# Kernel optimization log

Measured on AMD Instinct MI355X. Metric: run time of the kernel, lower is better.

The kernel has to match this reference:

```python
import jax, jax.numpy as jnp
import numpy as np

N = 50000      # nodes
E = 800000     # edges (avg degree 16)
B = 8          # graphs in batch
HID = 64       # hidden channels
NCLS = 40
EPS = 1e-5     # BatchNorm eps


def _init(key, shape, fan_in):
    return jax.random.normal(key, shape, dtype=jnp.float32) / np.sqrt(fan_in)


def setup_inputs() -> dict:
    key = jax.random.key(0)
    ks = jax.random.split(key, 12)
    d = {}
    d["x"] = jax.random.normal(ks[0], (N, 3), jnp.float32)
    d["pos"] = jax.random.normal(ks[1], (N, 3), jnp.float32)
    d["edge_attr"] = jax.random.normal(ks[2], (E,), jnp.float32)
    d["edge_index"] = jax.random.randint(ks[3], (2, E), 0, N, dtype=jnp.int32)
    d["batch"] = jnp.sort(jax.random.randint(ks[4], (N,), 0, B, dtype=jnp.int32))
    # conv1 MLP: input = edge_attr(1) + (x_j - x_i)(6) + x_i(6) = 13, two Lin->ReLU->BN blocks
    d1 = 13
    d["c1_W0"] = _init(ks[5], (d1, HID), d1); d["c1_b0"] = jnp.zeros((HID,), jnp.float32)
    d["c1_g0"] = jnp.ones((HID,), jnp.float32); d["c1_be0"] = jnp.zeros((HID,), jnp.float32)
    d["c1_W1"] = _init(ks[6], (HID, HID), HID); d["c1_b1"] = jnp.zeros((HID,), jnp.float32)
    d["c1_g1"] = jnp.ones((HID,), jnp.float32); d["c1_be1"] = jnp.zeros((HID,), jnp.float32)
    # 3 CustomEdgeConvWeighted layers, MLP input = 2*(3+HID) = 134; stacked over layer dim
    L = 3; dw = 2 * (3 + HID)
    d["cw_W0"] = _init(ks[7], (L, dw, HID), dw); d["cw_b0"] = jnp.zeros((L, HID), jnp.float32)
    d["cw_g0"] = jnp.ones((L, HID), jnp.float32); d["cw_be0"] = jnp.zeros((L, HID), jnp.float32)
    d["cw_W1"] = _init(ks[8], (L, HID, HID), HID); d["cw_b1"] = jnp.zeros((L, HID), jnp.float32)
    d["cw_g1"] = jnp.ones((L, HID), jnp.float32); d["cw_be1"] = jnp.zeros((L, HID), jnp.float32)
    # classifier head: jump-cat of 4 pooled layer outputs -> 4*HID
    d["lin1_W"] = _init(ks[9], (4 * HID, HID), 4 * HID); d["lin1_b"] = jnp.zeros((HID,), jnp.float32)
    d["lin2_W"] = _init(ks[10], (HID, NCLS), HID); d["lin2_b"] = jnp.zeros((NCLS,), jnp.float32)
    return d


def _mlp_layer(h, W, b, g, be):
    # Lin -> ReLU -> BatchNorm1d (training-mode batch stats)
    h = jax.nn.relu(h @ W + b)
    mu = h.mean(axis=0)
    var = h.var(axis=0)
    return (h - mu) * jax.lax.rsqrt(var + EPS) * g + be


def _edge_conv(x, pos, src, dst, extra, p0, p1):
    xc = jnp.concatenate([pos, x], axis=1)        # [N, 3+C]
    xi = xc[dst]                                   # target features  [E, 3+C]
    xj = xc[src]                                   # source features  [E, 3+C]
    parts = [xj - xi, xi]
    if extra is not None:
        parts = [extra] + parts                    # cat([edge_attr, x_j - x_i, x_i])
    m = jnp.concatenate(parts, axis=-1)
    m = _mlp_layer(m, *p0)
    m = _mlp_layer(m, *p1)
    agg = jax.ops.segment_max(m, dst, num_segments=N)  # scatter-max aggregation
    return jnp.where(jnp.isfinite(agg), agg, 0.0)      # isolated nodes -> 0


def _mean_pool(x, batch):
    s = jax.ops.segment_sum(x, batch, num_segments=B)
    cnt = jax.ops.segment_sum(jnp.ones((x.shape[0],), x.dtype), batch, num_segments=B)
    return s / jnp.maximum(cnt, 1.0)[:, None]


def reference(x, pos, edge_attr, edge_index, batch,
              c1_W0, c1_b0, c1_g0, c1_be0, c1_W1, c1_b1, c1_g1, c1_be1,
              cw_W0, cw_b0, cw_g0, cw_be0, cw_W1, cw_b1, cw_g1, cw_be1,
              lin1_W, lin1_b, lin2_W, lin2_b):
    src, dst = edge_index[0], edge_index[1]
    h = jax.nn.relu(_edge_conv(x, pos, src, dst, edge_attr[:, None],
                               (c1_W0, c1_b0, c1_g0, c1_be0),
                               (c1_W1, c1_b1, c1_g1, c1_be1)))
    xs = [_mean_pool(h, batch)]
    for l in range(3):  # fixed small layer count
        h = jax.nn.relu(_edge_conv(h, pos, src, dst, None,
                                   (cw_W0[l], cw_b0[l], cw_g0[l], cw_be0[l]),
                                   (cw_W1[l], cw_b1[l], cw_g1[l], cw_be1[l])))
        xs.append(_mean_pool(h, batch))
    j = jnp.concatenate(xs, axis=-1)               # JumpingKnowledge 'cat' -> [B, 4*HID]
    z = jax.nn.relu(j @ lin1_W + lin1_b) @ lin2_W + lin2_b
    return jax.nn.log_softmax(z, axis=-1)
```

## Files before the change

### kernel.cpp

```cpp
#include <hip/hip_runtime.h>

#define EPSV 1e-5f

typedef __attribute__((ext_vector_type(8))) short bf16x8;
typedef __attribute__((ext_vector_type(4))) float f32x4;

__device__ inline unsigned short f2bf(float f){
    unsigned u = __float_as_uint(f);
    u += 0x7fffu + ((u >> 16) & 1u);
    return (unsigned short)(u >> 16);
}
__device__ inline float bf2f(unsigned short v){
    return __uint_as_float(((unsigned)v) << 16);
}
__device__ inline unsigned cvtpk(float a, float b){
    unsigned r;
    asm("v_cvt_pk_bf16_f32 %0, %1, %2" : "=v"(r) : "v"(a), "v"(b));
    return r;
}


__global__ void k_init(int* deg, int* cursor, int N, int* counters,
                       float* stats, int statsN, float* pool, int poolN,
                       float* nmax, int* src_pad, float* ea_pad, int G16){
    int total = max(N*64, G16);
    for (int i = blockIdx.x*blockDim.x + threadIdx.x; i < total; i += gridDim.x*blockDim.x){
        if (i < N*64) nmax[i] = 0.f;
        if (i < G16){ src_pad[i] = 0; ea_pad[i] = 0.f; }
        if (i < N){ deg[i] = 0; cursor[i] = 0; }
        if (i < 8) counters[i] = 0;
        if (i < statsN) stats[i] = 0.f;
        if (i < poolN)  pool[i]  = 0.f;
    }
}

__global__ void k_hist(const int* dst, int E, int* deg){
    for (int e = blockIdx.x*blockDim.x + threadIdx.x; e < E; e += gridDim.x*blockDim.x)
        atomicAdd(&deg[dst[e]], 1);
}

__global__ __launch_bounds__(256) void k_alloc(const int* __restrict__ deg, int N,
        int* __restrict__ gstart, int* counters){
    int lane = threadIdx.x & 63;
    for (int n = blockIdx.x*blockDim.x + threadIdx.x; n - lane < N; n += gridDim.x*blockDim.x){
        int d = (n < N) ? deg[n] : 0;
        int g = (d + 15) >> 4;
        int sg = g;
        for (int off = 1; off < 64; off <<= 1){
            int tg = __shfl_up(sg, off);
            if (lane >= off) sg += tg;
        }
        int bg = 0;
        if (lane == 63) bg = atomicAdd(&counters[1], sg);
        bg = __shfl(bg, 63);
        if (n < N) gstart[n] = bg + sg - g;
    }
}

__global__ void k_grpfill(const int* deg, const int* gstart, int N,
                          unsigned* grp_nv, const int* counters){
    if (blockIdx.x == 0 && threadIdx.x < 16)
        grp_nv[counters[1] + threadIdx.x] = 0u;
    for (int n = blockIdx.x*blockDim.x + threadIdx.x; n < N; n += gridDim.x*blockDim.x){
        int dg = deg[n];
        int g0 = gstart[n];
        int ng = (dg + 15) >> 4;
        for (int j = 0; j < ng; j++)
            grp_nv[g0 + j] = (unsigned)((n << 5) | min(dg - j*16, 16));
    }
}

__global__ void k_scatter(const int* src, const int* dst, const float* ea, int E,
                          const int* gstart, int* cursor, int* src_c, float* ea_c){
    for (int e = blockIdx.x*blockDim.x + threadIdx.x; e < E; e += gridDim.x*blockDim.x){
        int d = dst[e];
        int p = gstart[d]*16 + atomicAdd(&cursor[d], 1);
        src_c[p] = src[e];
        ea_c[p] = ea[e];
    }
}

__global__ void k_bounds(const int* batch, int N, int B, int* bstart){
    for (int n = blockIdx.x*blockDim.x + threadIdx.x; n < N; n += gridDim.x*blockDim.x){
        if (n == 0){ int b0 = batch[0]; for (int bb = 0; bb <= b0; bb++) bstart[bb] = 0; }
        int b1 = batch[n];
        int b2 = (n + 1 < N) ? batch[n + 1] : B;
        for (int bb = b1 + 1; bb <= b2; bb++) bstart[bb] = n + 1;
    }
}

__global__ __launch_bounds__(256) void k_fold(const float* __restrict__ sum0,
        const float* __restrict__ sq0, float invE,
        const float* __restrict__ g0, const float* __restrict__ be0,
        const float* __restrict__ W1f, const float* __restrict__ b1,
        unsigned short* __restrict__ w1sT, float* __restrict__ badd){
    __shared__ float a0s[64], c0s[64];
    int t = threadIdx.x;
    if (t < 64){
        float m = sum0[t]*invE;
        float v = fmaxf(sq0[t]*invE - m*m, 0.f);
        float r = rsqrtf(v + EPSV);
        float a = g0[t]*r;
        a0s[t] = a; c0s[t] = be0[t] - m*a;
    }
    __syncthreads();
    for (int i = t; i < 4096; i += 256){
        int n = i >> 6, k = i & 63;
        w1sT[i] = f2bf(a0s[k] * W1f[k*64 + n]);
    }
    if (t < 64){
        float acc = b1[t];
        for (int k = 0; k < 64; k++) acc = fmaf(c0s[k], W1f[k*64 + t], acc);
        badd[t] = acc;
    }
}


__global__ __launch_bounds__(256) void k_nodeproj(const float* __restrict__ pos,
        const float* __restrict__ feat, int F, const float* __restrict__ W,
        int ra, int rb, const float* __restrict__ b0,
        unsigned short* __restrict__ P, unsigned short* __restrict__ Q, int N){
    __shared__ float sWa[67*64];
    __shared__ float sWd[67*64];
    int D = 3 + F;
    for (int i = threadIdx.x; i < D*64; i += 256){
        int k = i >> 6, c = i & 63;
        float wa = W[(ra + k)*64 + c];
        sWa[i] = wa;
        sWd[i] = W[(rb + k)*64 + c] - wa;
    }
    __syncthreads();
    int lane = threadIdx.x & 63;
    int wid = (blockIdx.x*256 + threadIdx.x) >> 6;
    int nw  = (gridDim.x*256) >> 6;
    float bb = b0[lane];
    for (int n = wid; n < N; n += nw){
        float p = 0.f, q = 0.f;
        for (int k = 0; k < 3; k++){
            float v = pos[n*3 + k];
            p = fmaf(v, sWa[k*64 + lane], p);
            q = fmaf(v, sWd[k*64 + lane], q);
        }
        for (int k = 0; k < F; k++){
            float v = feat[n*F + k];
            p = fmaf(v, sWa[(3+k)*64 + lane], p);
            q = fmaf(v, sWd[(3+k)*64 + lane], q);
        }
        P[(size_t)n*64 + lane] = f2bf(p);
        Q[(size_t)n*64 + lane] = f2bf(q + bb);
    }
}

#define UNPACK_ADD(up, uq, pre0, pre1) \
    pre0 = __uint_as_float((up) << 16) + __uint_as_float((uq) << 16); \
    pre1 = __uint_as_float((up) & 0xffff0000u) + __uint_as_float((uq) & 0xffff0000u);

template<bool EA>
__global__ __launch_bounds__(256, 3) void k_statsA(const unsigned short* __restrict__ Pb,
        const unsigned short* __restrict__ Qb,
        const int* __restrict__ src_c, const float* __restrict__ ea_c,
        const float* __restrict__ w0e,
        const unsigned* __restrict__ grp_nv, const int* __restrict__ counters,
        float* sum0, float* sq0){
    int lane = threadIdx.x & 63;
    int lo = lane & 15, hi = lane >> 4;
    int wid = (blockIdx.x*256 + threadIdx.x) >> 6;
    int nwv = (gridDim.x*256) >> 6;
    float w0v[16];
    if (EA){
#pragma unroll
        for (int j = 0; j < 8; j++){
            w0v[j]   = w0e[hi*8 + j];
            w0v[8+j] = w0e[32 + hi*8 + j];
        }
    }
    float st1[16], st2[16];
#pragma unroll
    for (int j = 0; j < 16; j++){ st1[j] = 0.f; st2[j] = 0.f; }

    int NG = counters[1];
    int C  = (NG + nwv - 1) / nwv;
    int gw0 = wid * C;
    int cnum = min(C, NG - gw0);
    if (cnum > 0){
        unsigned mr[8]; int sr[8]; float er[8];
        uint4 pa[4], pb[4], qa[4], qb[4];
#pragma unroll
        for (int k = 0; k < 8; k++){
            int G = gw0 + k;
            mr[k] = grp_nv[G];
            sr[k] = src_c[(size_t)G*16 + lo];
            if (EA) er[k] = ea_c[(size_t)G*16 + lo];
        }
#pragma unroll
        for (int d = 0; d < 4; d++){
            const uint4* P4 = (const uint4*)(Pb + (size_t)sr[d]*64);
            const uint4* Q4 = (const uint4*)(Qb + (size_t)(mr[d] >> 5)*64);
            pa[d] = P4[hi]; pb[d] = P4[4+hi]; qa[d] = Q4[hi]; qb[d] = Q4[4+hi];
        }
        int itmax = (cnum + 7) & ~7;
        for (int it = 0; it < itmax; it += 8){
#pragma unroll
            for (int j = 0; j < 8; j++){
                int G = gw0 + it + j;
                unsigned mv = mr[j];
                float eav_all = EA ? er[j] : 0.f;
                int vcv = (it + j < cnum) ? (int)(mv & 31u) : 0;
                mr[j] = grp_nv[G + 8];
                sr[j] = src_c[(size_t)(G + 8)*16 + lo];
                if (EA) er[j] = ea_c[(size_t)(G + 8)*16 + lo];
                int d = j & 3;
                uint4 cpa = pa[d], cpb = pb[d], cqa = qa[d], cqb = qb[d];
                {
                    int s4 = sr[(j+4)&7]; unsigned m4 = mr[(j+4)&7];
                    const uint4* P4 = (const uint4*)(Pb + (size_t)s4*64);
                    const uint4* Q4 = (const uint4*)(Qb + (size_t)(m4 >> 5)*64);
                    pa[d] = P4[hi]; pb[d] = P4[4+hi]; qa[d] = Q4[hi]; qb[d] = Q4[4+hi];
                }
                bool vv = lo < vcv;
                float eav = (EA && vv) ? eav_all : 0.f;
#pragma unroll
                for (int w = 0; w < 4; w++){
                    float pre0, pre1;
                    UNPACK_ADD(((const unsigned*)&cpa)[w], ((const unsigned*)&cqa)[w], pre0, pre1);
                    if (EA){ pre0 = fmaf(eav, w0v[2*w], pre0); pre1 = fmaf(eav, w0v[2*w+1], pre1); }
                    float h0f = vv ? fmaxf(pre0, 0.f) : 0.f;
                    float h1f = vv ? fmaxf(pre1, 0.f) : 0.f;
                    st1[2*w]   += h0f; st2[2*w]   = fmaf(h0f, h0f, st2[2*w]);
                    st1[2*w+1] += h1f; st2[2*w+1] = fmaf(h1f, h1f, st2[2*w+1]);
                    UNPACK_ADD(((const unsigned*)&cpb)[w], ((const unsigned*)&cqb)[w], pre0, pre1);
                    if (EA){ pre0 = fmaf(eav, w0v[8+2*w], pre0); pre1 = fmaf(eav, w0v[8+2*w+1], pre1); }
                    h0f = vv ? fmaxf(pre0, 0.f) : 0.f;
                    h1f = vv ? fmaxf(pre1, 0.f) : 0.f;
                    st1[8+2*w]   += h0f; st2[8+2*w]   = fmaf(h0f, h0f, st2[8+2*w]);
                    st1[8+2*w+1] += h1f; st2[8+2*w+1] = fmaf(h1f, h1f, st2[8+2*w+1]);
                }
            }
        }
    }
#pragma unroll
    for (int m = 1; m < 16; m <<= 1){
#pragma unroll
        for (int j = 0; j < 16; j++){
            st1[j] += __shfl_xor(st1[j], m);
            st2[j] += __shfl_xor(st2[j], m);
        }
    }
    __shared__ float red[4*128];
    int w = threadIdx.x >> 6;
    if (lo == 0){
#pragma unroll
        for (int j = 0; j < 8; j++){
            red[w*128 + hi*8 + j]        = st1[j];
            red[w*128 + 32 + hi*8 + j]   = st1[8+j];
            red[w*128 + 64 + hi*8 + j]   = st2[j];
            red[w*128 + 96 + hi*8 + j]   = st2[8+j];
        }
    }
    __syncthreads();
    int t = threadIdx.x;
    if (t < 128){
        float v = red[t] + red[128 + t] + red[256 + t] + red[384 + t];
        if (t < 64) atomicAdd(&sum0[t], v);
        else        atomicAdd(&sq0[t - 64], v);
    }
}

template<bool EA>
__global__ __launch_bounds__(256, 2) void k_passB2(
        const unsigned short* __restrict__ Pb, const unsigned short* __restrict__ Qb,
        const int* __restrict__ src_c, const float* __restrict__ ea_c,
        const float* __restrict__ w0e,
        const unsigned* __restrict__ grp_nv, const int* __restrict__ counters,
        const unsigned short* __restrict__ w1sT, const float* __restrict__ badd,
        float* nmax, float* sum1, float* sq1){
    int lane = threadIdx.x & 63;
    int lo = lane & 15, hi = lane >> 4;
    int wid = (blockIdx.x*256 + threadIdx.x) >> 6;
    int nwv = (gridDim.x*256) >> 6;

    float w0v[16];
    if (EA){
#pragma unroll
        for (int j = 0; j < 8; j++){
            w0v[j]   = w0e[hi*8 + j];
            w0v[8+j] = w0e[32 + hi*8 + j];
        }
    }
    bf16x8 bfr[2][4];
#pragma unroll
    for (int ks = 0; ks < 2; ks++)
#pragma unroll
        for (int nt = 0; nt < 4; nt++)
            bfr[ks][nt] = *(const bf16x8*)(w1sT + (size_t)(nt*16 + lo)*64 + ks*32 + hi*8);
    float baddv[4];
#pragma unroll
    for (int nt = 0; nt < 4; nt++) baddv[nt] = badd[nt*16 + lo];

    float st1[4] = {0.f,0.f,0.f,0.f}, st2[4] = {0.f,0.f,0.f,0.f};
    int NG = counters[1];
    int C  = (NG + nwv - 1) / nwv;
    int gw0 = wid * C;
    int cnum = min(C, NG - gw0);
    if (cnum > 0){
        unsigned mr[8]; int sr[8]; float er[8];
        uint4 pa[4], pb[4], qa[4], qb[4];
#pragma unroll
        for (int k = 0; k < 8; k++){
            int G = gw0 + k;
            mr[k] = grp_nv[G];
            sr[k] = src_c[(size_t)G*16 + lo];
            if (EA) er[k] = ea_c[(size_t)G*16 + lo];
        }
#pragma unroll
        for (int d = 0; d < 4; d++){
            const uint4* P4 = (const uint4*)(Pb + (size_t)sr[d]*64);
            const uint4* Q4 = (const uint4*)(Qb + (size_t)(mr[d] >> 5)*64);
            pa[d] = P4[hi]; pb[d] = P4[4+hi]; qa[d] = Q4[hi]; qb[d] = Q4[4+hi];
        }
        int itmax = (cnum + 7) & ~7;
        for (int it = 0; it < itmax; it += 8){
#pragma unroll
            for (int j = 0; j < 8; j++){
                int G = gw0 + it + j;
                unsigned mv = mr[j];
                float eav_all = EA ? er[j] : 0.f;
                int vcv = (it + j < cnum) ? (int)(mv & 31u) : 0;
                mr[j] = grp_nv[G + 8];
                sr[j] = src_c[(size_t)(G + 8)*16 + lo];
                if (EA) er[j] = ea_c[(size_t)(G + 8)*16 + lo];
                int d = j & 3;
                uint4 cpa = pa[d], cpb = pb[d], cqa = qa[d], cqb = qb[d];
                {
                    int s4 = sr[(j+4)&7]; unsigned m4 = mr[(j+4)&7];
                    const uint4* P4 = (const uint4*)(Pb + (size_t)s4*64);
                    const uint4* Q4 = (const uint4*)(Qb + (size_t)(m4 >> 5)*64);
                    pa[d] = P4[hi]; pb[d] = P4[4+hi]; qa[d] = Q4[hi]; qb[d] = Q4[4+hi];
                }
                if (vcv > 0){
                    bool vv = lo < vcv;
                    float eav = (EA && vv) ? eav_all : 0.f;
                    bf16x8 af0, af1;
#pragma unroll
                    for (int w = 0; w < 4; w++){
                        float pre0, pre1;
                        UNPACK_ADD(((const unsigned*)&cpa)[w], ((const unsigned*)&cqa)[w], pre0, pre1);
                        if (EA){ pre0 = fmaf(eav, w0v[2*w], pre0); pre1 = fmaf(eav, w0v[2*w+1], pre1); }
                        ((unsigned*)&af0)[w] = cvtpk(fmaxf(pre0, 0.f), fmaxf(pre1, 0.f));
                        UNPACK_ADD(((const unsigned*)&cpb)[w], ((const unsigned*)&cqb)[w], pre0, pre1);
                        if (EA){ pre0 = fmaf(eav, w0v[8+2*w], pre0); pre1 = fmaf(eav, w0v[8+2*w+1], pre1); }
                        ((unsigned*)&af1)[w] = cvtpk(fmaxf(pre0, 0.f), fmaxf(pre1, 0.f));
                    }
                    f32x4 acc[4];
#pragma unroll
                    for (int nt = 0; nt < 4; nt++){
                        acc[nt] = (f32x4){0.f, 0.f, 0.f, 0.f};
                        acc[nt] = __builtin_amdgcn_mfma_f32_16x16x32_bf16(af0, bfr[0][nt], acc[nt], 0, 0, 0);
                        acc[nt] = __builtin_amdgcn_mfma_f32_16x16x32_bf16(af1, bfr[1][nt], acc[nt], 0, 0, 0);
                    }
                    int n = (int)(mv >> 5);
#pragma unroll
                    for (int nt = 0; nt < 4; nt++){
                        float m = 0.f;
#pragma unroll
                        for (int r = 0; r < 4; r++){
                            float h = ((hi*4 + r) < vcv) ? fmaxf(acc[nt][r] + baddv[nt], 0.f) : 0.f;
                            st1[nt] += h;
                            st2[nt] = fmaf(h, h, st2[nt]);
                            m = fmaxf(m, h);
                        }
                        m = fmaxf(m, __shfl_xor(m, 16));
                        m = fmaxf(m, __shfl_xor(m, 32));
                        if (lane < 16)
                            atomicMax((unsigned int*)&nmax[(size_t)n*64 + nt*16 + lane], __float_as_uint(m));
                    }
                }
            }
        }
    }
#pragma unroll
    for (int nt = 0; nt < 4; nt++){
        st1[nt] += __shfl_xor(st1[nt], 16); st1[nt] += __shfl_xor(st1[nt], 32);
        st2[nt] += __shfl_xor(st2[nt], 16); st2[nt] += __shfl_xor(st2[nt], 32);
    }
    __shared__ float red[4*128];
    int w = threadIdx.x >> 6;
    if (lane < 16){
#pragma unroll
        for (int nt = 0; nt < 4; nt++){
            red[w*128 + nt*16 + lane]      = st1[nt];
            red[w*128 + 64 + nt*16 + lane] = st2[nt];
        }
    }
    __syncthreads();
    int t = threadIdx.x;
    if (t < 128){
        float v = red[t] + red[128 + t] + red[256 + t] + red[384 + t];
        if (t < 64) atomicAdd(&sum1[t], v);
        else        atomicAdd(&sq1[t - 64], v);
    }
}

template<bool PROJ>
__global__ __launch_bounds__(256) void k_finproj(float* __restrict__ nmax,
        const int* __restrict__ deg,
        const float* __restrict__ sum1, const float* __restrict__ sq1, float invE,
        const float* __restrict__ g1, const float* __restrict__ be1,
        const int* __restrict__ batch,
        const float* __restrict__ pos, const float* __restrict__ W, const float* __restrict__ b0n,
        unsigned short* __restrict__ P, unsigned short* __restrict__ Q,
        float* pooll, int N, int B){
    __shared__ float sWa[67*64];
    __shared__ float sWd[67*64];
    if (PROJ){
        for (int i = threadIdx.x; i < 67*64; i += 256){
            int k = i >> 6, c = i & 63;
            float wa = W[k*64 + c];
            sWa[i] = wa;
            sWd[i] = W[(67 + k)*64 + c] - wa;
        }
        __syncthreads();
    }
    int lane = threadIdx.x & 63;
    float m1 = sum1[lane]*invE;
    float v1 = fmaxf(sq1[lane]*invE - m1*m1, 0.f);
    float r1 = rsqrtf(v1 + EPSV);
    float av = g1[lane]*r1;
    float cv = be1[lane] - m1*av;
    float bb = PROJ ? b0n[lane] : 0.f;
    int wid = (blockIdx.x*256 + threadIdx.x) >> 6;
    int nw  = (gridDim.x*256) >> 6;
    int chunk = (N + nw - 1) / nw;
    int n0 = wid * chunk, n1 = min(n0 + chunk, N);
    int rep = wid & 7;
    float run = 0.f; int curb = -1;
    for (int n = n0; n < n1; n++){
        size_t idx = (size_t)n*64 + lane;
        float mv = nmax[idx];
        nmax[idx] = 0.f;
        float val = (deg[n] > 0) ? fmaxf(fmaf(av, mv, cv), 0.f) : 0.f;
        int b = batch[n];
        if (b != curb){
            if (curb >= 0) atomicAdd(&pooll[(rep*B + curb)*64 + lane], run);
            run = 0.f; curb = b;
        }
        run += val;
        if (PROJ){
            float p = 0.f, q = 0.f;
            for (int k = 0; k < 3; k++){
                float v = pos[n*3 + k];
                p = fmaf(v, sWa[k*64 + lane], p);
                q = fmaf(v, sWd[k*64 + lane], q);
            }
#pragma unroll
            for (int k = 0; k < 64; k++){
                float v = __shfl(val, k);
                p = fmaf(v, sWa[(3+k)*64 + lane], p);
                q = fmaf(v, sWd[(3+k)*64 + lane], q);
            }
            P[idx] = f2bf(p);
            Q[idx] = f2bf(q + bb);
        }
    }
    if (curb >= 0) atomicAdd(&pooll[(rep*B + curb)*64 + lane], run);
}

__global__ __launch_bounds__(512) void k_head(const float* __restrict__ pool, const int* __restrict__ bstart,
        const float* __restrict__ l1W, const float* __restrict__ l1b,
        const float* __restrict__ l2W, const float* __restrict__ l2b,
        float* __restrict__ out, int B, int NCLS){
    __shared__ float js[8*256];
    __shared__ float z1[8*64];
    __shared__ float zs[8*40];
    int t = threadIdx.x;
    for (int i = t; i < B*256; i += 512){
        int b = i >> 8, k = i & 255;
        int l = k >> 6, c = k & 63;
        float s = 0.f;
        for (int r = 0; r < 8; r++) s += pool[((l*8 + r)*B + b)*64 + c];
        float cnt = (float)(bstart[b+1] - bstart[b]);
        js[b*256 + k] = s / fmaxf(cnt, 1.f);
    }
    __syncthreads();
    for (int i = t; i < B*64; i += 512){
        int b = i >> 6, c = i & 63;
        float acc = l1b[c];
        for (int k = 0; k < 256; k++) acc = fmaf(js[b*256 + k], l1W[k*64 + c], acc);
        z1[i] = fmaxf(acc, 0.f);
    }
    __syncthreads();
    for (int i = t; i < B*NCLS; i += 512){
        int b = i / NCLS, c = i - b*NCLS;
        float acc = l2b[c];
        for (int k = 0; k < 64; k++) acc = fmaf(z1[b*64 + k], l2W[k*NCLS + c], acc);
        zs[b*NCLS + c] = acc;
    }
    __syncthreads();
    if (t < B){
        float m = -1e30f;
        for (int c = 0; c < NCLS; c++) m = fmaxf(m, zs[t*NCLS + c]);
        float se = 0.f;
        for (int c = 0; c < NCLS; c++) se += expf(zs[t*NCLS + c] - m);
        float lse = m + logf(se);
        for (int c = 0; c < NCLS; c++) out[t*NCLS + c] = zs[t*NCLS + c] - lse;
    }
}


extern "C" void kernel_launch(void* const* d_in, const int* in_sizes, int n_in,
                              void* d_out, int out_size, void* d_ws, size_t ws_size,
                              hipStream_t stream){
    const float* x      = (const float*)d_in[0];
    const float* pos    = (const float*)d_in[1];
    const float* eattr  = (const float*)d_in[2];
    const int*   eidx   = (const int*)d_in[3];
    const int*   batch  = (const int*)d_in[4];
    const float* c1_W0  = (const float*)d_in[5];
    const float* c1_b0  = (const float*)d_in[6];
    const float* c1_g0  = (const float*)d_in[7];
    const float* c1_be0 = (const float*)d_in[8];
    const float* c1_W1  = (const float*)d_in[9];
    const float* c1_b1  = (const float*)d_in[10];
    const float* c1_g1  = (const float*)d_in[11];
    const float* c1_be1 = (const float*)d_in[12];
    const float* cw_W0  = (const float*)d_in[13];
    const float* cw_b0  = (const float*)d_in[14];
    const float* cw_g0  = (const float*)d_in[15];
    const float* cw_be0 = (const float*)d_in[16];
    const float* cw_W1  = (const float*)d_in[17];
    const float* cw_b1  = (const float*)d_in[18];
    const float* cw_g1  = (const float*)d_in[19];
    const float* cw_be1 = (const float*)d_in[20];
    const float* lin1_W = (const float*)d_in[21];
    const float* lin1_b = (const float*)d_in[22];
    const float* lin2_W = (const float*)d_in[23];
    const float* lin2_b = (const float*)d_in[24];
    float* out = (float*)d_out;

    int N = in_sizes[0] / 3;
    int E = in_sizes[2];
    int NCLS = in_sizes[24];
    int B = out_size / NCLS;
    const int* src = eidx;
    const int* dst = eidx + E;

    char* w = (char*)d_ws;
    auto alloc = [&](size_t bytes) -> char* {
        char* p = w;
        w += (bytes + 255) & ~(size_t)255;
        return p;
    };
    int Gmax = E/16 + N + 32;
    int G16  = Gmax*16;
    unsigned short* P = (unsigned short*)alloc((size_t)N*64*2);
    unsigned short* Q = (unsigned short*)alloc((size_t)N*64*2);
    float* nmax     = (float*)alloc((size_t)N*64*4);
    int*   deg      = (int*)alloc((size_t)N*4);
    int*   gstart   = (int*)alloc((size_t)(N+1)*4);
    int*   cursor   = (int*)alloc((size_t)N*4);
    int*   src_c    = (int*)alloc((size_t)G16*4);
    float* ea_c     = (float*)alloc((size_t)G16*4);
    unsigned* grp_nv = (unsigned*)alloc((size_t)Gmax*4);
    int*   counters = (int*)alloc(256);
    int*   bstart   = (int*)alloc((size_t)(B+1)*4);
    float* stats    = (float*)alloc(4*256*4);
    unsigned short* w1sT = (unsigned short*)alloc(4096*2);
    float* badd     = (float*)alloc(64*4);
    float* pool     = (float*)alloc((size_t)4*8*B*64*4);

    float invE = 1.f / (float)E;
    int eblocks = (E + 255) / 256;
    int nblocks = (N + 255) / 256;

    k_init<<<2048, 256, 0, stream>>>(deg, cursor, N, counters, stats, 4*256, pool, 4*8*B*64,
                                     nmax, src_c, ea_c, G16);
    k_hist<<<eblocks, 256, 0, stream>>>(dst, E, deg);
    k_alloc<<<nblocks, 256, 0, stream>>>(deg, N, gstart, counters);
    k_grpfill<<<nblocks, 256, 0, stream>>>(deg, gstart, N, grp_nv, counters);
    k_scatter<<<eblocks, 256, 0, stream>>>(src, dst, eattr, E, gstart, cursor, src_c, ea_c);
    k_bounds<<<nblocks, 256, 0, stream>>>(batch, N, B, bstart);

    k_nodeproj<<<512, 256, 0, stream>>>(pos, x, 3, c1_W0, 1, 7, c1_b0, P, Q, N);

    for (int l = 0; l < 4; l++){
        const float* g0  = (l == 0) ? c1_g0  : cw_g0  + (l-1)*64;
        const float* be0 = (l == 0) ? c1_be0 : cw_be0 + (l-1)*64;
        const float* W1f = (l == 0) ? c1_W1  : cw_W1  + (size_t)(l-1)*4096;
        const float* b1  = (l == 0) ? c1_b1  : cw_b1  + (l-1)*64;
        const float* g1  = (l == 0) ? c1_g1  : cw_g1  + (l-1)*64;
        const float* be1 = (l == 0) ? c1_be1 : cw_be1 + (l-1)*64;
        float* sum0 = stats + l*256;       float* sq0 = sum0 + 64;
        float* sum1 = sum0 + 128;          float* sq1 = sum0 + 192;
        float* pooll = pool + (size_t)l*8*B*64;

        if (l == 0){
            k_statsA<true><<<1024, 256, 0, stream>>>(P, Q, src_c, ea_c, c1_W0, grp_nv,
                                                     counters, sum0, sq0);
            k_fold<<<1, 256, 0, stream>>>(sum0, sq0, invE, g0, be0, W1f, b1, w1sT, badd);
            k_passB2<true><<<1024, 256, 0, stream>>>(P, Q, src_c, ea_c, c1_W0, grp_nv, counters,
                                                     w1sT, badd, nmax, sum1, sq1);
        } else {
            k_statsA<false><<<1024, 256, 0, stream>>>(P, Q, src_c, nullptr, nullptr, grp_nv,
                                                      counters, sum0, sq0);
            k_fold<<<1, 256, 0, stream>>>(sum0, sq0, invE, g0, be0, W1f, b1, w1sT, badd);
            k_passB2<false><<<1024, 256, 0, stream>>>(P, Q, src_c, nullptr, nullptr, grp_nv, counters,
                                                      w1sT, badd, nmax, sum1, sq1);
        }
        if (l < 3)
            k_finproj<true><<<512, 256, 0, stream>>>(nmax, deg, sum1, sq1, invE, g1, be1, batch,
                                                     pos, cw_W0 + (size_t)l*134*64, cw_b0 + l*64,
                                                     P, Q, pooll, N, B);
        else
            k_finproj<false><<<256, 256, 0, stream>>>(nmax, deg, sum1, sq1, invE, g1, be1, batch,
                                                      pos, nullptr, nullptr,
                                                      P, Q, pooll, N, B);
    }

    k_head<<<1, 512, 0, stream>>>(pool, bstart, lin1_W, lin1_b, lin2_W, lin2_b, out, B, NCLS);
}
```

Measured before the change: 743.6 us.

## Pack src index and bf16 edge attr into one word; fold BN into passB2

Source index (16 bits) and edge attribute (bf16) are packed into a single 32-bit word per edge slot. This halves the per-edge index/attr loads in the stats and MLP passes and the scatter writes. The scatter is split into 8 group-range slices across blocks to localize writes. The separate single-block fold kernel is removed: each wave in passB2 recomputes the BN-folded W1 fragments and bias directly from the stats. This saves four launches but adds redundant per-wave work, and it rounds edge_attr to bf16 and assumes N < 65536.

```diff
diff --git a/kernel.cpp b/kernel.cpp
--- a/kernel.cpp
+++ b/kernel.cpp
@@ -22,11 +22,11 @@
 
 __global__ void k_init(int* deg, int* cursor, int N, int* counters,
                        float* stats, int statsN, float* pool, int poolN,
-                       float* nmax, int* src_pad, float* ea_pad, int G16){
+                       float* nmax, unsigned* edge_p, int G16){
     int total = max(N*64, G16);
     for (int i = blockIdx.x*blockDim.x + threadIdx.x; i < total; i += gridDim.x*blockDim.x){
         if (i < N*64) nmax[i] = 0.f;
-        if (i < G16){ src_pad[i] = 0; ea_pad[i] = 0.f; }
+        if (i < G16) edge_p[i] = 0u;
         if (i < N){ deg[i] = 0; cursor[i] = 0; }
         if (i < 8) counters[i] = 0;
         if (i < statsN) stats[i] = 0.f;
@@ -70,13 +70,23 @@
     }
 }
 
-__global__ void k_scatter(const int* src, const int* dst, const float* ea, int E,
-                          const int* gstart, int* cursor, int* src_c, float* ea_c){
-    for (int e = blockIdx.x*blockDim.x + threadIdx.x; e < E; e += gridDim.x*blockDim.x){
+__global__ __launch_bounds__(256) void k_scatter(const int* __restrict__ src,
+        const int* __restrict__ dst, const float* __restrict__ ea, int E,
+        const int* __restrict__ gstart, int* cursor, unsigned* __restrict__ edge_p,
+        const int* __restrict__ counters){
+    int NG = counters[1];
+    int per = (NG + 7) >> 3;
+    int slice = blockIdx.x & 7;
+    int glo = slice * per, ghi = glo + per;
+    int bslice = blockIdx.x >> 3;
+    int nbs = gridDim.x >> 3;
+    for (int e = bslice*blockDim.x + threadIdx.x; e < E; e += nbs*blockDim.x){
         int d = dst[e];
-        int p = gstart[d]*16 + atomicAdd(&cursor[d], 1);
-        src_c[p] = src[e];
-        ea_c[p] = ea[e];
+        int g = gstart[d];
+        if (g >= glo && g < ghi){
+            int p = g*16 + atomicAdd(&cursor[d], 1);
+            edge_p[p] = ((unsigned)f2bf(ea[e]) << 16) | (unsigned)src[e];
+        }
     }
 }
 
@@ -86,32 +96,6 @@
         int b1 = batch[n];
         int b2 = (n + 1 < N) ? batch[n + 1] : B;
         for (int bb = b1 + 1; bb <= b2; bb++) bstart[bb] = n + 1;
-    }
-}
-
-__global__ __launch_bounds__(256) void k_fold(const float* __restrict__ sum0,
-        const float* __restrict__ sq0, float invE,
-        const float* __restrict__ g0, const float* __restrict__ be0,
-        const float* __restrict__ W1f, const float* __restrict__ b1,
-        unsigned short* __restrict__ w1sT, float* __restrict__ badd){
-    __shared__ float a0s[64], c0s[64];
-    int t = threadIdx.x;
-    if (t < 64){
-        float m = sum0[t]*invE;
-        float v = fmaxf(sq0[t]*invE - m*m, 0.f);
-        float r = rsqrtf(v + EPSV);
-        float a = g0[t]*r;
-        a0s[t] = a; c0s[t] = be0[t] - m*a;
-    }
-    __syncthreads();
-    for (int i = t; i < 4096; i += 256){
-        int n = i >> 6, k = i & 63;
-        w1sT[i] = f2bf(a0s[k] * W1f[k*64 + n]);
-    }
-    if (t < 64){
-        float acc = b1[t];
-        for (int k = 0; k < 64; k++) acc = fmaf(c0s[k], W1f[k*64 + t], acc);
-        badd[t] = acc;
     }
 }
 
@@ -158,8 +142,7 @@
 template<bool EA>
 __global__ __launch_bounds__(256, 3) void k_statsA(const unsigned short* __restrict__ Pb,
         const unsigned short* __restrict__ Qb,
-        const int* __restrict__ src_c, const float* __restrict__ ea_c,
-        const float* __restrict__ w0e,
+        const unsigned* __restrict__ edge_p, const float* __restrict__ w0e,
         const unsigned* __restrict__ grp_nv, const int* __restrict__ counters,
         float* sum0, float* sq0){
     int lane = threadIdx.x & 63;
@@ -183,18 +166,17 @@
     int gw0 = wid * C;
     int cnum = min(C, NG - gw0);
     if (cnum > 0){
-        unsigned mr[8]; int sr[8]; float er[8];
+        unsigned mr[8]; unsigned pr[8];
         uint4 pa[4], pb[4], qa[4], qb[4];
 #pragma unroll
         for (int k = 0; k < 8; k++){
             int G = gw0 + k;
             mr[k] = grp_nv[G];
-            sr[k] = src_c[(size_t)G*16 + lo];
-            if (EA) er[k] = ea_c[(size_t)G*16 + lo];
+            pr[k] = edge_p[(size_t)G*16 + lo];
         }
 #pragma unroll
         for (int d = 0; d < 4; d++){
-            const uint4* P4 = (const uint4*)(Pb + (size_t)sr[d]*64);
+            const uint4* P4 = (const uint4*)(Pb + (size_t)(pr[d] & 0xffffu)*64);
             const uint4* Q4 = (const uint4*)(Qb + (size_t)(mr[d] >> 5)*64);
             pa[d] = P4[hi]; pb[d] = P4[4+hi]; qa[d] = Q4[hi]; qb[d] = Q4[4+hi];
         }
@@ -204,21 +186,20 @@
             for (int j = 0; j < 8; j++){
                 int G = gw0 + it + j;
                 unsigned mv = mr[j];
-                float eav_all = EA ? er[j] : 0.f;
+                unsigned pv = pr[j];
                 int vcv = (it + j < cnum) ? (int)(mv & 31u) : 0;
                 mr[j] = grp_nv[G + 8];
-                sr[j] = src_c[(size_t)(G + 8)*16 + lo];
-                if (EA) er[j] = ea_c[(size_t)(G + 8)*16 + lo];
+                pr[j] = edge_p[(size_t)(G + 8)*16 + lo];
                 int d = j & 3;
                 uint4 cpa = pa[d], cpb = pb[d], cqa = qa[d], cqb = qb[d];
                 {
-                    int s4 = sr[(j+4)&7]; unsigned m4 = mr[(j+4)&7];
-                    const uint4* P4 = (const uint4*)(Pb + (size_t)s4*64);
+                    unsigned p4 = pr[(j+4)&7]; unsigned m4 = mr[(j+4)&7];
+                    const uint4* P4 = (const uint4*)(Pb + (size_t)(p4 & 0xffffu)*64);
                     const uint4* Q4 = (const uint4*)(Qb + (size_t)(m4 >> 5)*64);
                     pa[d] = P4[hi]; pb[d] = P4[4+hi]; qa[d] = Q4[hi]; qb[d] = Q4[4+hi];
                 }
                 bool vv = lo < vcv;
-                float eav = (EA && vv) ? eav_all : 0.f;
+                float eav = (EA && vv) ? bf2f((unsigned short)(pv >> 16)) : 0.f;
 #pragma unroll
                 for (int w = 0; w < 4; w++){
                     float pre0, pre1;
@@ -269,10 +250,11 @@
 template<bool EA>
 __global__ __launch_bounds__(256, 2) void k_passB2(
         const unsigned short* __restrict__ Pb, const unsigned short* __restrict__ Qb,
-        const int* __restrict__ src_c, const float* __restrict__ ea_c,
-        const float* __restrict__ w0e,
+        const unsigned* __restrict__ edge_p, const float* __restrict__ w0e,
         const unsigned* __restrict__ grp_nv, const int* __restrict__ counters,
-        const unsigned short* __restrict__ w1sT, const float* __restrict__ badd,
+        const float* __restrict__ sum0, const float* __restrict__ sq0, float invE,
+        const float* __restrict__ g0, const float* __restrict__ be0,
+        const float* __restrict__ W1f, const float* __restrict__ b1,
         float* nmax, float* sum1, float* sq1){
     int lane = threadIdx.x & 63;
     int lo = lane & 15, hi = lane >> 4;
@@ -288,14 +270,40 @@
         }
     }
     bf16x8 bfr[2][4];
-#pragma unroll
-    for (int ks = 0; ks < 2; ks++)
-#pragma unroll
-        for (int nt = 0; nt < 4; nt++)
-            bfr[ks][nt] = *(const bf16x8*)(w1sT + (size_t)(nt*16 + lo)*64 + ks*32 + hi*8);
     float baddv[4];
-#pragma unroll
-    for (int nt = 0; nt < 4; nt++) baddv[nt] = badd[nt*16 + lo];
+    {
+        float a0v[16], c0v[16];
+#pragma unroll
+        for (int j = 0; j < 8; j++){
+            int ch = hi*8 + j, ch2 = 32 + ch;
+            float m  = sum0[ch]*invE;
+            float vv = fmaxf(sq0[ch]*invE - m*m, 0.f);
+            float r  = rsqrtf(vv + EPSV);
+            a0v[j] = g0[ch]*r;  c0v[j] = be0[ch] - m*a0v[j];
+            float m2  = sum0[ch2]*invE;
+            float vv2 = fmaxf(sq0[ch2]*invE - m2*m2, 0.f);
+            float r2  = rsqrtf(vv2 + EPSV);
+            a0v[8+j] = g0[ch2]*r2;  c0v[8+j] = be0[ch2] - m2*a0v[8+j];
+        }
+        float crow[4] = {0.f,0.f,0.f,0.f};
+#pragma unroll
+        for (int ks = 0; ks < 2; ks++)
+#pragma unroll
+            for (int nt = 0; nt < 4; nt++)
+#pragma unroll
+                for (int j = 0; j < 8; j++){
+                    int k = ks*32 + hi*8 + j;
+                    float wv = W1f[k*64 + nt*16 + lo];
+                    crow[nt] = fmaf(c0v[ks*8+j], wv, crow[nt]);
+                    bfr[ks][nt][j] = (short)f2bf(a0v[ks*8+j] * wv);
+                }
+#pragma unroll
+        for (int nt = 0; nt < 4; nt++){
+            crow[nt] += __shfl_xor(crow[nt], 16);
+            crow[nt] += __shfl_xor(crow[nt], 32);
+            baddv[nt] = b1[nt*16 + lo] + crow[nt];
+        }
+    }
 
     float st1[4] = {0.f,0.f,0.f,0.f}, st2[4] = {0.f,0.f,0.f,0.f};
     int NG = counters[1];
@@ -303,18 +311,17 @@
     int gw0 = wid * C;
     int cnum = min(C, NG - gw0);
     if (cnum > 0){
-        unsigned mr[8]; int sr[8]; float er[8];
+        unsigned mr[8]; unsigned pr[8];
         uint4 pa[4], pb[4], qa[4], qb[4];
 #pragma unroll
         for (int k = 0; k < 8; k++){
             int G = gw0 + k;
             mr[k] = grp_nv[G];
-            sr[k] = src_c[(size_t)G*16 + lo];
-            if (EA) er[k] = ea_c[(size_t)G*16 + lo];
+            pr[k] = edge_p[(size_t)G*16 + lo];
         }
 #pragma unroll
         for (int d = 0; d < 4; d++){
-            const uint4* P4 = (const uint4*)(Pb + (size_t)sr[d]*64);
+            const uint4* P4 = (const uint4*)(Pb + (size_t)(pr[d] & 0xffffu)*64);
             const uint4* Q4 = (const uint4*)(Qb + (size_t)(mr[d] >> 5)*64);
             pa[d] = P4[hi]; pb[d] = P4[4+hi]; qa[d] = Q4[hi]; qb[d] = Q4[4+hi];
         }
@@ -324,22 +331,21 @@
             for (int j = 0; j < 8; j++){
                 int G = gw0 + it + j;
                 unsigned mv = mr[j];
-                float eav_all = EA ? er[j] : 0.f;
+                unsigned pv = pr[j];
                 int vcv = (it + j < cnum) ? (int)(mv & 31u) : 0;
                 mr[j] = grp_nv[G + 8];
-                sr[j] = src_c[(size_t)(G + 8)*16 + lo];
-                if (EA) er[j] = ea_c[(size_t)(G + 8)*16 + lo];
+                pr[j] = edge_p[(size_t)(G + 8)*16 + lo];
                 int d = j & 3;
                 uint4 cpa = pa[d], cpb = pb[d], cqa = qa[d], cqb = qb[d];
                 {
-                    int s4 = sr[(j+4)&7]; unsigned m4 = mr[(j+4)&7];
-                    const uint4* P4 = (const uint4*)(Pb + (size_t)s4*64);
+                    unsigned p4 = pr[(j+4)&7]; unsigned m4 = mr[(j+4)&7];
+                    const uint4* P4 = (const uint4*)(Pb + (size_t)(p4 & 0xffffu)*64);
                     const uint4* Q4 = (const uint4*)(Qb + (size_t)(m4 >> 5)*64);
                     pa[d] = P4[hi]; pb[d] = P4[4+hi]; qa[d] = Q4[hi]; qb[d] = Q4[4+hi];
                 }
                 if (vcv > 0){
                     bool vv = lo < vcv;
-                    float eav = (EA && vv) ? eav_all : 0.f;
+                    float eav = (EA && vv) ? bf2f((unsigned short)(pv >> 16)) : 0.f;
                     bf16x8 af0, af1;
 #pragma unroll
                     for (int w = 0; w < 4; w++){
@@ -558,14 +564,11 @@
     int*   deg      = (int*)alloc((size_t)N*4);
     int*   gstart   = (int*)alloc((size_t)(N+1)*4);
     int*   cursor   = (int*)alloc((size_t)N*4);
-    int*   src_c    = (int*)alloc((size_t)G16*4);
-    float* ea_c     = (float*)alloc((size_t)G16*4);
+    unsigned* edge_p = (unsigned*)alloc((size_t)G16*4);
     unsigned* grp_nv = (unsigned*)alloc((size_t)Gmax*4);
     int*   counters = (int*)alloc(256);
     int*   bstart   = (int*)alloc((size_t)(B+1)*4);
     float* stats    = (float*)alloc(4*256*4);
-    unsigned short* w1sT = (unsigned short*)alloc(4096*2);
-    float* badd     = (float*)alloc(64*4);
     float* pool     = (float*)alloc((size_t)4*8*B*64*4);
 
     float invE = 1.f / (float)E;
@@ -573,11 +576,11 @@
     int nblocks = (N + 255) / 256;
 
     k_init<<<2048, 256, 0, stream>>>(deg, cursor, N, counters, stats, 4*256, pool, 4*8*B*64,
-                                     nmax, src_c, ea_c, G16);
+                                     nmax, edge_p, G16);
     k_hist<<<eblocks, 256, 0, stream>>>(dst, E, deg);
     k_alloc<<<nblocks, 256, 0, stream>>>(deg, N, gstart, counters);
     k_grpfill<<<nblocks, 256, 0, stream>>>(deg, gstart, N, grp_nv, counters);
-    k_scatter<<<eblocks, 256, 0, stream>>>(src, dst, eattr, E, gstart, cursor, src_c, ea_c);
+    k_scatter<<<1024, 256, 0, stream>>>(src, dst, eattr, E, gstart, cursor, edge_p, counters);
     k_bounds<<<nblocks, 256, 0, stream>>>(batch, N, B, bstart);
 
     k_nodeproj<<<512, 256, 0, stream>>>(pos, x, 3, c1_W0, 1, 7, c1_b0, P, Q, N);
@@ -594,17 +597,17 @@
         float* pooll = pool + (size_t)l*8*B*64;
 
         if (l == 0){
-            k_statsA<true><<<1024, 256, 0, stream>>>(P, Q, src_c, ea_c, c1_W0, grp_nv,
+            k_statsA<true><<<1024, 256, 0, stream>>>(P, Q, edge_p, c1_W0, grp_nv,
                                                      counters, sum0, sq0);
-            k_fold<<<1, 256, 0, stream>>>(sum0, sq0, invE, g0, be0, W1f, b1, w1sT, badd);
-            k_passB2<true><<<1024, 256, 0, stream>>>(P, Q, src_c, ea_c, c1_W0, grp_nv, counters,
-                                                     w1sT, badd, nmax, sum1, sq1);
+            k_passB2<true><<<1024, 256, 0, stream>>>(P, Q, edge_p, c1_W0, grp_nv, counters,
+                                                     sum0, sq0, invE, g0, be0, W1f, b1,
+                                                     nmax, sum1, sq1);
         } else {
-            k_statsA<false><<<1024, 256, 0, stream>>>(P, Q, src_c, nullptr, nullptr, grp_nv,
+            k_statsA<false><<<1024, 256, 0, stream>>>(P, Q, edge_p, nullptr, grp_nv,
                                                       counters, sum0, sq0);
-            k_fold<<<1, 256, 0, stream>>>(sum0, sq0, invE, g0, be0, W1f, b1, w1sT, badd);
-            k_passB2<false><<<1024, 256, 0, stream>>>(P, Q, src_c, nullptr, nullptr, grp_nv, counters,
-                                                      w1sT, badd, nmax, sum1, sq1);
+            k_passB2<false><<<1024, 256, 0, stream>>>(P, Q, edge_p, nullptr, grp_nv, counters,
+                                                      sum0, sq0, invE, g0, be0, W1f, b1,
+                                                      nmax, sum1, sq1);
         }
         if (l < 3)
             k_finproj<true><<<512, 256, 0, stream>>>(nmax, deg, sum1, sq1, invE, g1, be1, batch,
```

Result: faster. 725.2 us (-2.5%).
